# Performance work log

Hardware: AMD Instinct MI355X
Metric: run time of the kernel (lower is better)

## Reference

```python
import jax, jax.numpy as jnp
import numpy as np


def make_blur():
    # 5x5x5 separable binomial kernel, normalized to sum 1 then scaled by 8
    k = np.asarray([1, 4, 6, 4, 1], dtype=np.float32)
    k3 = k[:, None, None] * k[None, :, None] * k[None, None, :]
    k3 = k3 / k3.sum() * 8.0
    return jnp.asarray(k3.reshape(1, 1, 5, 5, 5))


def setup_inputs() -> dict:
    key = jax.random.key(0)
    N, C, D, H, W = 2, 32, 48, 48, 48
    x = jax.random.normal(key, (N, C, D, H, W), dtype=jnp.float32)
    return {
        "x": x,
        "blur": make_blur(),
        "output_shape": (N, C, 2 * D, 2 * H, 2 * W),
    }


def reference(x, blur, output_shape):
    N, C, D, H, W = x.shape
    # torch: output_padding[i] = output_shape[i+2] - ((x.shape[i+2]-1)*2 + 1)
    op = tuple(int(output_shape[i + 2]) - ((x.shape[i + 2] - 1) * 2 + 1) for i in range(3))
    pad = blur.shape[-1] // 4  # = 1
    # depthwise: fold channels into batch, single-channel conv
    xr = x.reshape(N * C, 1, D, H, W)
    # replicate pad by 1 on each spatial side (torch F.pad mode='replicate')
    xr = jnp.pad(xr, ((0, 0), (0, 0), (pad, pad), (pad, pad), (pad, pad)), mode='edge')
    # conv_transpose3d(stride=2, padding=4*pad=4, output_padding=op) is equivalent to a
    # conv with lhs_dilation=2 and per-dim padding (k-1-4, k-1-4+op) = (0, op),
    # using the spatially flipped kernel (the binomial kernel is symmetric anyway).
    kern = blur[:, :, ::-1, ::-1, ::-1]
    y = jax.lax.conv_general_dilated(
        xr, kern,
        window_strides=(1, 1, 1),
        padding=[(0, op[0]), (0, op[1]), (0, op[2])],
        lhs_dilation=(2, 2, 2),
        dimension_numbers=('NCDHW', 'OIDHW', 'NCDHW'))
    return y.reshape(N, C, int(output_shape[2]), int(output_shape[3]), int(output_shape[4]))
```

## Files before the change

### kernel.cpp

```cpp
#include <hip/hip_runtime.h>


typedef float f32x4 __attribute__((ext_vector_type(4)));

constexpr int DIN = 48, HIN = 48, WIN = 48;
constexpr int HW = HIN * WIN;
constexpr int DOUT = 96, HOUT = 96, WOUT = 96;
constexpr int NC = 64;
constexpr int THREADS = NC * 24 * 24 * 24;

__global__ __launch_bounds__(256) void Upsample2x2x2_kernel(
    const float* __restrict__ x, float* __restrict__ out)
{
    int idx = blockIdx.x * 256 + threadIdx.x;
    int t   = idx % 24;
    int tmp = idx / 24;
    int b0h = tmp % 24;
    tmp    /= 24;
    int a0h = tmp % 24;
    int nc  = tmp / 24;

    const int a0 = a0h * 2, b0 = b0h * 2, w0 = t * 2;
    const float* __restrict__ xb = x + (size_t)nc * (DIN * HW);

    const int ai[4] = { a0 > 0 ? a0 - 1 : 0, a0, a0 + 1,
                        a0 + 2 < DIN ? a0 + 2 : DIN - 1 };
    const int bi[4] = { b0 > 0 ? b0 - 1 : 0, b0, b0 + 1,
                        b0 + 2 < HIN ? b0 + 2 : HIN - 1 };
    const int wm = w0 > 0 ? w0 - 1 : 0;
    const int wp = w0 + 2 < WIN ? w0 + 2 : WIN - 1;

    float r[4][4][4];
    #pragma unroll
    for (int i = 0; i < 4; i++) {
        const float* __restrict__ xd = xb + ai[i] * HW;
        #pragma unroll
        for (int j = 0; j < 4; j++) {
            const float* __restrict__ row = xd + bi[j] * WIN;
            float2 m = *reinterpret_cast<const float2*>(row + w0);
            float u0 = row[wm];
            float u3 = row[wp];
            float u1 = m.x, u2 = m.y;
            r[i][j][0] = fmaf(6.f, u1, u0) + u2;
            r[i][j][1] = u1 + u2;
            r[i][j][2] = fmaf(6.f, u2, u1) + u3;
            r[i][j][3] = u2 + u3;
        }
    }

    float* __restrict__ ob = out + (size_t)nc * (DOUT * HOUT * WOUT);
    const size_t obase = ((size_t)(a0 * 2) * HOUT + (b0 * 2)) * WOUT + t * 4;

    #pragma unroll
    for (int win = 0; win < 2; win++) {
        float He[4][4], Ho[4][4];
        #pragma unroll
        for (int i = 0; i < 4; i++)
            #pragma unroll
            for (int k = 0; k < 4; k++) {
                He[i][k] = fmaf(6.f, r[i][win + 1][k], r[i][win][k]) + r[i][win + 2][k];
                Ho[i][k] = r[i][win + 1][k] + r[i][win + 2][k];
            }

        #pragma unroll
        for (int ap = 0; ap < 2; ap++) {
            float vee[4], voe[4], veo[4], voo[4];
            #pragma unroll
            for (int k = 0; k < 4; k++) {
                vee[k] = fmaf(6.f, He[ap + 1][k], He[ap][k]) + He[ap + 2][k];
                voe[k] = He[ap + 1][k] + He[ap + 2][k];
                veo[k] = fmaf(6.f, Ho[ap + 1][k], Ho[ap][k]) + Ho[ap + 2][k];
                voo[k] = Ho[ap + 1][k] + Ho[ap + 2][k];
            }
            size_t rbase = obase + ((size_t)(ap * 2) * HOUT + win * 2) * WOUT;
            f32x4 s0 = { vee[0] * (1.f/512), vee[1] * (1.f/128),
                         vee[2] * (1.f/512), vee[3] * (1.f/128) };
            f32x4 s1 = { veo[0] * (1.f/128), veo[1] * (1.f/32),
                         veo[2] * (1.f/128), veo[3] * (1.f/32) };
            f32x4 s2 = { voe[0] * (1.f/128), voe[1] * (1.f/32),
                         voe[2] * (1.f/128), voe[3] * (1.f/32) };
            f32x4 s3 = { voo[0] * (1.f/32),  voo[1] * (1.f/8),
                         voo[2] * (1.f/32),  voo[3] * (1.f/8) };
            __builtin_nontemporal_store(s0, reinterpret_cast<f32x4*>(ob + rbase));
            __builtin_nontemporal_store(s1, reinterpret_cast<f32x4*>(ob + rbase + WOUT));
            __builtin_nontemporal_store(s2, reinterpret_cast<f32x4*>(ob + rbase + (size_t)HOUT * WOUT));
            __builtin_nontemporal_store(s3, reinterpret_cast<f32x4*>(ob + rbase + (size_t)HOUT * WOUT + WOUT));
        }
    }
}

extern "C" void kernel_launch(void* const* d_in, const int* in_sizes, int n_in,
                              void* d_out, int out_size, void* d_ws, size_t ws_size,
                              hipStream_t stream) {
    const float* x = (const float*)d_in[0];
    float* out = (float*)d_out;
    int blocks = THREADS / 256;
    Upsample2x2x2_kernel<<<blocks, 256, 0, stream>>>(x, out);
}
```

Before: 47.79 us.

## Interleave per-plane row filtering with output stores to shrink register pressure

The loop is restructured so each depth plane's W-filtered values are reduced right away into H-filtered partials. The first output stores are issued as soon as three planes are ready, instead of after all 64 values are held live. Index arithmetic moves from 64-bit size_t to 32-bit int, and launch bounds now request 4 blocks per CU. The aim is fewer VGPRs, higher occupancy and earlier store issue, at the cost of relying on 32-bit offsets fitting, which they do for these sizes.

```diff
diff --git a/kernel.cpp b/kernel.cpp
--- a/kernel.cpp
+++ b/kernel.cpp
@@ -5,11 +5,12 @@
 
 constexpr int DIN = 48, HIN = 48, WIN = 48;
 constexpr int HW = HIN * WIN;
-constexpr int DOUT = 96, HOUT = 96, WOUT = 96;
+constexpr int HOUT = 96, WOUT = 96;
+constexpr int PS = HOUT * WOUT;
 constexpr int NC = 64;
 constexpr int THREADS = NC * 24 * 24 * 24;
 
-__global__ __launch_bounds__(256) void Upsample2x2x2_kernel(
+__global__ __launch_bounds__(256, 4) void Upsample2x2x2_kernel(
     const float* __restrict__ x, float* __restrict__ out)
 {
     int idx = blockIdx.x * 256 + threadIdx.x;
@@ -21,7 +22,7 @@
     int nc  = tmp / 24;
 
     const int a0 = a0h * 2, b0 = b0h * 2, w0 = t * 2;
-    const float* __restrict__ xb = x + (size_t)nc * (DIN * HW);
+    const float* __restrict__ xb = x + nc * (DIN * HW);
 
     const int ai[4] = { a0 > 0 ? a0 - 1 : 0, a0, a0 + 1,
                         a0 + 2 < DIN ? a0 + 2 : DIN - 1 };
@@ -30,10 +31,16 @@
     const int wm = w0 > 0 ? w0 - 1 : 0;
     const int wp = w0 + 2 < WIN ? w0 + 2 : WIN - 1;
 
-    float r[4][4][4];
+    float* __restrict__ ob = out + nc * (2 * DIN * PS);
+    const int obase = (a0 * 2 * HOUT + b0 * 2) * WOUT + t * 4;
+
+    float He[4][2][4], Ho[4][2][4];
+
     #pragma unroll
     for (int i = 0; i < 4; i++) {
         const float* __restrict__ xd = xb + ai[i] * HW;
+
+        float rr[4][4];
         #pragma unroll
         for (int j = 0; j < 4; j++) {
             const float* __restrict__ row = xd + bi[j] * WIN;
@@ -41,50 +48,46 @@
             float u0 = row[wm];
             float u3 = row[wp];
             float u1 = m.x, u2 = m.y;
-            r[i][j][0] = fmaf(6.f, u1, u0) + u2;
-            r[i][j][1] = u1 + u2;
-            r[i][j][2] = fmaf(6.f, u2, u1) + u3;
-            r[i][j][3] = u2 + u3;
+            rr[j][0] = fmaf(6.f, u1, u0) + u2;
+            rr[j][1] = u1 + u2;
+            rr[j][2] = fmaf(6.f, u2, u1) + u3;
+            rr[j][3] = u2 + u3;
         }
-    }
 
-    float* __restrict__ ob = out + (size_t)nc * (DOUT * HOUT * WOUT);
-    const size_t obase = ((size_t)(a0 * 2) * HOUT + (b0 * 2)) * WOUT + t * 4;
-
-    #pragma unroll
-    for (int win = 0; win < 2; win++) {
-        float He[4][4], Ho[4][4];
         #pragma unroll
-        for (int i = 0; i < 4; i++)
+        for (int win = 0; win < 2; win++)
             #pragma unroll
             for (int k = 0; k < 4; k++) {
-                He[i][k] = fmaf(6.f, r[i][win + 1][k], r[i][win][k]) + r[i][win + 2][k];
-                Ho[i][k] = r[i][win + 1][k] + r[i][win + 2][k];
+                He[i][win][k] = fmaf(6.f, rr[win + 1][k], rr[win][k]) + rr[win + 2][k];
+                Ho[i][win][k] = rr[win + 1][k] + rr[win + 2][k];
             }
 
-        #pragma unroll
-        for (int ap = 0; ap < 2; ap++) {
-            float vee[4], voe[4], veo[4], voo[4];
+        if (i >= 2) {
+            const int ap = i - 2;
             #pragma unroll
-            for (int k = 0; k < 4; k++) {
-                vee[k] = fmaf(6.f, He[ap + 1][k], He[ap][k]) + He[ap + 2][k];
-                voe[k] = He[ap + 1][k] + He[ap + 2][k];
-                veo[k] = fmaf(6.f, Ho[ap + 1][k], Ho[ap][k]) + Ho[ap + 2][k];
-                voo[k] = Ho[ap + 1][k] + Ho[ap + 2][k];
+            for (int win = 0; win < 2; win++) {
+                float vee[4], voe[4], veo[4], voo[4];
+                #pragma unroll
+                for (int k = 0; k < 4; k++) {
+                    vee[k] = fmaf(6.f, He[ap + 1][win][k], He[ap][win][k]) + He[ap + 2][win][k];
+                    voe[k] = He[ap + 1][win][k] + He[ap + 2][win][k];
+                    veo[k] = fmaf(6.f, Ho[ap + 1][win][k], Ho[ap][win][k]) + Ho[ap + 2][win][k];
+                    voo[k] = Ho[ap + 1][win][k] + Ho[ap + 2][win][k];
+                }
+                const int rbase = obase + ap * 2 * PS + win * 2 * WOUT;
+                f32x4 s0 = { vee[0] * (1.f/512), vee[1] * (1.f/128),
+                             vee[2] * (1.f/512), vee[3] * (1.f/128) };
+                f32x4 s1 = { veo[0] * (1.f/128), veo[1] * (1.f/32),
+                             veo[2] * (1.f/128), veo[3] * (1.f/32) };
+                f32x4 s2 = { voe[0] * (1.f/128), voe[1] * (1.f/32),
+                             voe[2] * (1.f/128), voe[3] * (1.f/32) };
+                f32x4 s3 = { voo[0] * (1.f/32),  voo[1] * (1.f/8),
+                             voo[2] * (1.f/32),  voo[3] * (1.f/8) };
+                __builtin_nontemporal_store(s0, reinterpret_cast<f32x4*>(ob + rbase));
+                __builtin_nontemporal_store(s1, reinterpret_cast<f32x4*>(ob + rbase + WOUT));
+                __builtin_nontemporal_store(s2, reinterpret_cast<f32x4*>(ob + rbase + PS));
+                __builtin_nontemporal_store(s3, reinterpret_cast<f32x4*>(ob + rbase + PS + WOUT));
             }
-            size_t rbase = obase + ((size_t)(ap * 2) * HOUT + win * 2) * WOUT;
-            f32x4 s0 = { vee[0] * (1.f/512), vee[1] * (1.f/128),
-                         vee[2] * (1.f/512), vee[3] * (1.f/128) };
-            f32x4 s1 = { veo[0] * (1.f/128), veo[1] * (1.f/32),
-                         veo[2] * (1.f/128), veo[3] * (1.f/32) };
-            f32x4 s2 = { voe[0] * (1.f/128), voe[1] * (1.f/32),
-                         voe[2] * (1.f/128), voe[3] * (1.f/32) };
-            f32x4 s3 = { voo[0] * (1.f/32),  voo[1] * (1.f/8),
-                         voo[2] * (1.f/32),  voo[3] * (1.f/8) };
-            __builtin_nontemporal_store(s0, reinterpret_cast<f32x4*>(ob + rbase));
-            __builtin_nontemporal_store(s1, reinterpret_cast<f32x4*>(ob + rbase + WOUT));
-            __builtin_nontemporal_store(s2, reinterpret_cast<f32x4*>(ob + rbase + (size_t)HOUT * WOUT));
-            __builtin_nontemporal_store(s3, reinterpret_cast<f32x4*>(ob + rbase + (size_t)HOUT * WOUT + WOUT));
         }
     }
 }
```

Measured after the change: 48.16 us. Within noise of the previous version (+0.8%).
